# Kernel tuning notes

Hardware: AMD Instinct MI355X
Metric: run time of the kernel (lower is better)

Reference implementation:

```python
import jax, jax.numpy as jnp
import numpy as np

MIN_SPAN = 3
MAX_SPAN = 20
LEN_BONUS = 0.01
LN_EPS = 1e-5


def setup_inputs() -> dict:
    key = jax.random.key(0)
    ks = jax.random.split(key, 10)
    B, S, H = 16, 2048, 1024
    D = H // 2
    hidden_states = jax.random.normal(ks[0], (B, S, H), dtype=jnp.float32)
    lengths = jax.random.randint(ks[1], (B,), S // 2, S + 1)
    attention_mask = (jnp.arange(S)[None, :] < lengths[:, None]).astype(jnp.int32)
    return {
        'hidden_states': hidden_states,
        'attention_mask': attention_mask,
        'Wq': 0.02 * jax.random.normal(ks[2], (H, D), dtype=jnp.float32),
        'bq': jnp.zeros((D,), jnp.float32),
        'Wk': 0.02 * jax.random.normal(ks[3], (H, D), dtype=jnp.float32),
        'bk': jnp.zeros((D,), jnp.float32),
        'W1': 0.02 * jax.random.normal(ks[4], (H, D), dtype=jnp.float32),
        'b1': jnp.zeros((D,), jnp.float32),
        'ln_g': jnp.ones((D,), jnp.float32),
        'ln_b': jnp.zeros((D,), jnp.float32),
        'W2': 0.01 * jax.random.normal(ks[5], (D, 1), dtype=jnp.float32),
        'b2': jnp.zeros((1,), jnp.float32),
    }


def _token_scores(hidden_states, mask, Wq, bq, Wk, bk, W1, b1, ln_g, ln_b, W2, b2):
    q = hidden_states @ Wq + bq                      # [B,S,D]
    k = hidden_states @ Wk + bk                      # [B,S,D]
    d = q.shape[-1]
    scores = jnp.einsum('bsd,btd->bst', q, k) / jnp.sqrt(jnp.float32(d))
    scores = jnp.where(mask[:, None, :], scores, -10000.0)
    probs = jax.nn.softmax(scores, axis=-1)
    context = jnp.einsum('bst,bth->bsh', probs, hidden_states)  # [B,S,H]
    h = context @ W1 + b1
    mu = jnp.mean(h, axis=-1, keepdims=True)
    var = jnp.var(h, axis=-1, keepdims=True)
    h = (h - mu) * jax.lax.rsqrt(var + LN_EPS) * ln_g + ln_b
    h = jax.nn.relu(h)                               # dropout: eval mode -> identity
    ts = (h @ W2 + b2)[..., 0]                       # [B,S]
    return jnp.where(mask, ts, -10000.0)


def _rationale_mask(token_scores, mask):
    # Faithful to original: starts[0]==0 always, so prefix subtraction never
    # fires; span score = cumsum[start+L-1]/L + bonus. Argmax over (L asc, start asc)
    # with strict-greater updates == first max of the flattened (L, start) grid.
    B, S = token_scores.shape
    valid_len = jnp.sum(mask, axis=1)                # [B] int
    cum = jnp.cumsum(token_scores, axis=1)           # [B,S]
    L = jnp.arange(MIN_SPAN, MAX_SPAN + 1)           # [NL]
    starts = jnp.arange(S)                           # [S]
    end = jnp.clip(starts[None, :] + L[:, None] - 1, 0, S - 1)   # [NL,S]
    bonus = LEN_BONUS * (L.astype(jnp.float32) / MAX_SPAN)       # [NL]
    grid = cum[:, end] / L[None, :, None].astype(jnp.float32) + bonus[None, :, None]  # [B,NL,S]
    vl = valid_len[:, None, None]
    valid = (L[None, :, None] <= vl) & (starts[None, None, :] <= vl - L[None, :, None])
    grid = jnp.where(valid, grid, -jnp.inf)
    idx = jnp.argmax(grid.reshape(B, -1), axis=1)    # first max -> torch tie-break
    best_L = MIN_SPAN + idx // S
    best_s = idx % S
    pos = jnp.arange(S)[None, :]
    span = (pos >= best_s[:, None]) & (pos < (best_s + best_L)[:, None])
    short = (valid_len <= MIN_SPAN)[:, None]
    short_span = pos < valid_len[:, None]
    return jnp.where(short, short_span, span).astype(token_scores.dtype)


def reference(hidden_states, attention_mask, Wq, bq, Wk, bk, W1, b1, ln_g, ln_b, W2, b2):
    mask = attention_mask.astype(bool)
    token_scores = _token_scores(hidden_states, mask, Wq, bq, Wk, bk, W1, b1, ln_g, ln_b, W2, b2)
    rationale = _rationale_mask(token_scores, mask)
    token_probs = jax.nn.softmax(jnp.where(mask, token_scores, -10000.0), axis=-1)
    attended = hidden_states * rationale[:, :, None]
    lengths = jnp.sum(rationale, axis=1, keepdims=True) + 1e-6
    pooled = jnp.sum(attended, axis=1) / lengths
    return token_scores, rationale, token_probs, attended, pooled
```

## Files before the change

kernel.cpp:

```cpp
#include <hip/hip_runtime.h>

typedef _Float16 f16;
typedef __attribute__((ext_vector_type(8))) _Float16 f16x8;
typedef __attribute__((ext_vector_type(4))) _Float16 f16x4v;
typedef __attribute__((ext_vector_type(4))) float f32x4;

#define B_ 16
#define S_ 2048
#define H_ 1024
#define D_ 512

__device__ __forceinline__ void gload16(const f16* g, f16* l) {
  __builtin_amdgcn_global_load_lds(
      (const __attribute__((address_space(1))) unsigned int*)g,
      (__attribute__((address_space(3))) unsigned int*)l, 16, 0, 0);
}

__global__ __launch_bounds__(256) void cvt_hs_kernel(const float4* __restrict__ in,
                                                     f16x4v* __restrict__ out) {
  long long i = (long long)blockIdx.x * 256 + threadIdx.x;
  float4 v = in[i];
  f16x4v o = {(f16)v.x, (f16)v.y, (f16)v.z, (f16)v.w};
  out[i] = o;
}

__global__ __launch_bounds__(256) void build_wt_kernel(const float* __restrict__ Wq,
                                                       const float* __restrict__ Wk,
                                                       const float* __restrict__ W1,
                                                       f16* __restrict__ Wt) {
  int i = blockIdx.x * 256 + threadIdx.x;
  int n = i >> 10;
  int k = i & 1023;
  const float* src = (n < 512) ? Wq : ((n < 1024) ? Wk : W1);
  int nn = n & 511;
  Wt[i] = (f16)src[k * 512 + nn];
}

__global__ __launch_bounds__(256) void build_bias_kernel(const float* __restrict__ bq,
                                                         const float* __restrict__ bk,
                                                         float* __restrict__ bias) {
  int i = blockIdx.x * 256 + threadIdx.x;
  if (i < 1024) bias[i] = (i < 512) ? bq[i] : bk[i - 512];
}

__global__ __launch_bounds__(256) void lens_kernel(const int* __restrict__ mask,
                                                   int* __restrict__ lens) {
  int b = blockIdx.x;
  int tid = threadIdx.x;
  int s = 0;
  for (int c = tid; c < S_; c += 256) s += mask[b * S_ + c];
  __shared__ int r[256];
  r[tid] = s;
  __syncthreads();
  for (int o = 128; o > 0; o >>= 1) {
    if (tid < o) r[tid] += r[tid + o];
    __syncthreads();
  }
  if (tid == 0) lens[b] = r[0];
}

__global__ __launch_bounds__(256) void gemm_bt(
    const f16* __restrict__ A, const f16* __restrict__ Bm, void* __restrict__ Cout,
    int K, int lda, int ldb, int ldc,
    long long sA, long long sB, long long sC,
    float scale, const float* __restrict__ bias, int mode,
    const int* __restrict__ lens, int lflags) {
  const int bz = blockIdx.z;

  const int ntiles = gridDim.x, mtiles = gridDim.y;
  const int flat = blockIdx.y * ntiles + blockIdx.x;
  const int per = 8 * ntiles;
  const int grp = flat / per;
  const int rem = flat - grp * per;
  const int gbase = grp * 8;
  const int gsz = (mtiles - gbase) < 8 ? (mtiles - gbase) : 8;
  const int mt = gbase + rem % gsz;
  const int nt = rem / gsz;
  const int m0 = mt * 128;
  const int n0 = nt * 128;

  int Keff = K;
  if (lflags) {
    const int len = lens[(lflags & 1) ? (m0 >> 11) : bz];
    if ((lflags & 3) && (m0 & 2047) >= len) return;
    if ((lflags & 4) && n0 >= len) return;
    if (lflags & 8) { int kl = (len + 63) & ~63; Keff = kl < K ? kl : K; }
  }

  A += (long long)bz * sA;
  Bm += (long long)bz * sB;

  __shared__ f16 As[128 * 64];
  __shared__ f16 Bs[128 * 64];

  const int tid = threadIdx.x;
  const int lane = tid & 63;
  const int wid = tid >> 6;
  const int wm = wid & 1, wn = wid >> 1;

  f32x4 acc[4][4] = {};

  const int lr8 = lane >> 3;
  const int sg = lane & 7;

  for (int k0 = 0; k0 < Keff; k0 += 64) {
#pragma unroll
    for (int it = 0; it < 4; ++it) {
      const int r0 = it * 32 + wid * 8;
      const int r = r0 + lr8;
      const int cg = sg ^ (r & 7);
      gload16(A + (long long)(m0 + r) * lda + k0 + cg * 8, As + r0 * 64);
      gload16(Bm + (long long)(n0 + r) * ldb + k0 + cg * 8, Bs + r0 * 64);
    }
    __syncthreads();

#pragma unroll
    for (int kk = 0; kk < 64; kk += 32) {
      const int cg = (kk >> 3) + (lane >> 4);
      f16x8 af[4], bf[4];
#pragma unroll
      for (int i = 0; i < 4; ++i) {
        const int row = wm * 64 + i * 16 + (lane & 15);
        af[i] = *(const f16x8*)(As + row * 64 + ((cg ^ (row & 7)) << 3));
      }
#pragma unroll
      for (int j = 0; j < 4; ++j) {
        const int row = wn * 64 + j * 16 + (lane & 15);
        bf[j] = *(const f16x8*)(Bs + row * 64 + ((cg ^ (row & 7)) << 3));
      }
#pragma unroll
      for (int i = 0; i < 4; ++i)
#pragma unroll
        for (int j = 0; j < 4; ++j)
          acc[i][j] = __builtin_amdgcn_mfma_f32_16x16x32_f16(af[i], bf[j], acc[i][j], 0, 0, 0);
    }
    __syncthreads();
  }

  const long long cb = (long long)bz * sC;
  const int lr = ((lane >> 4) << 2);
  const int lc = lane & 15;
#pragma unroll
  for (int i = 0; i < 4; ++i) {
#pragma unroll
    for (int j = 0; j < 4; ++j) {
      const int col = n0 + wn * 64 + j * 16 + lc;
      const float bv = bias ? bias[col] : 0.0f;
      if (mode == 2) {
        const int rowb = m0 + wm * 64 + i * 16 + lr;
        const int b = rowb >> 11, t = rowb & 2047;
        f16x4v pk;
#pragma unroll
        for (int r = 0; r < 4; ++r) pk[r] = (f16)(acc[i][j][r] * scale + bv);
        *(f16x4v*)((f16*)Cout + ((long long)b << 20) + (long long)col * 2048 + t) = pk;
      } else {
#pragma unroll
        for (int r = 0; r < 4; ++r) {
          const int row = m0 + wm * 64 + i * 16 + lr + r;
          float v = acc[i][j][r] * scale + bv;
          if (mode == 1)
            ((f16*)Cout)[cb + (long long)row * ldc + col] = (f16)v;
          else
            ((float*)Cout)[cb + (long long)row * ldc + col] = v;
        }
      }
    }
  }
}

__global__ __launch_bounds__(256) void softmax_rows_kernel(f16* __restrict__ sc,
                                                           const int* __restrict__ lens) {
  const int tid = threadIdx.x;
  const int lane = tid & 63;
  const int row = blockIdx.x * 4 + (tid >> 6);
  const int len = lens[row >> 11];
  if ((row & 2047) >= ((len + 127) & ~127)) return;
  f16* p = sc + (long long)row * S_;

  f16x8 v[4];
#pragma unroll
  for (int c = 0; c < 4; ++c) v[c] = *(const f16x8*)(p + c * 512 + lane * 8);

  float m = -1e30f;
#pragma unroll
  for (int c = 0; c < 4; ++c)
#pragma unroll
    for (int j = 0; j < 8; ++j) {
      const int col = c * 512 + lane * 8 + j;
      if (col < len) m = fmaxf(m, (float)v[c][j]);
    }
#pragma unroll
  for (int o = 32; o > 0; o >>= 1) m = fmaxf(m, __shfl_xor(m, o, 64));

  float e[32];
  float s = 0.0f;
#pragma unroll
  for (int c = 0; c < 4; ++c)
#pragma unroll
    for (int j = 0; j < 8; ++j) {
      const int col = c * 512 + lane * 8 + j;
      const float x = (col < len) ? __expf((float)v[c][j] - m) : 0.0f;
      e[c * 8 + j] = x;
      s += x;
    }
#pragma unroll
  for (int o = 32; o > 0; o >>= 1) s += __shfl_xor(s, o, 64);
  const float inv = 1.0f / s;

#pragma unroll
  for (int c = 0; c < 4; ++c) {
    f16x8 w;
#pragma unroll
    for (int j = 0; j < 8; ++j) w[j] = (f16)(e[c * 8 + j] * inv);
    *(f16x8*)(p + c * 512 + lane * 8) = w;
  }
}

__global__ __launch_bounds__(256) void ln_score_kernel(
    const float* __restrict__ h, const int* __restrict__ lens,
    const float* __restrict__ g, const float* __restrict__ bt,
    const float* __restrict__ W2, const float* __restrict__ b2,
    float* __restrict__ ts, float* __restrict__ out_ts) {
  const int token = blockIdx.x;
  const float* hp = h + (long long)token * D_;
  const int tid = threadIdx.x;
  float x0 = hp[tid], x1 = hp[tid + 256];
  __shared__ float r1[256], r2[256];
  r1[tid] = x0 + x1;
  r2[tid] = x0 * x0 + x1 * x1;
  __syncthreads();
  for (int o = 128; o > 0; o >>= 1) {
    if (tid < o) { r1[tid] += r1[tid + o]; r2[tid] += r2[tid + o]; }
    __syncthreads();
  }
  const float mu = r1[0] * (1.0f / D_);
  const float var = r2[0] * (1.0f / D_) - mu * mu;
  const float rs = rsqrtf(var + 1e-5f);
  float y0 = fmaxf((x0 - mu) * rs * g[tid] + bt[tid], 0.0f);
  float y1 = fmaxf((x1 - mu) * rs * g[tid + 256] + bt[tid + 256], 0.0f);
  float d = y0 * W2[tid] + y1 * W2[tid + 256];
  __syncthreads();
  r1[tid] = d;
  __syncthreads();
  for (int o = 128; o > 0; o >>= 1) {
    if (tid < o) r1[tid] += r1[tid + o];
    __syncthreads();
  }
  if (tid == 0) {
    float v = r1[0] + b2[0];
    ts[token] = v;
    const int b = token >> 11, s = token & (S_ - 1);
    out_ts[token] = (s < lens[b]) ? v : -10000.0f;
  }
}

__global__ __launch_bounds__(256) void rationale_kernel(
    const float* __restrict__ ts, const int* __restrict__ lens,
    float* __restrict__ out_rat, int* __restrict__ span) {
  const int b = blockIdx.x;
  const int tid = threadIdx.x;
  const int len = lens[b];
  __shared__ float cum[S_];
  __shared__ float rbest[256];
  __shared__ int ridx[256];

  for (int s = tid; s < S_; s += 256)
    cum[s] = (s < len) ? ts[b * S_ + s] : -10000.0f;
  __syncthreads();
  if (tid == 0) {
    float a = 0.0f;
    for (int s = 0; s < S_; s += 4) {
      float4 v = *(float4*)(cum + s);
      a += v.x; v.x = a;
      a += v.y; v.y = a;
      a += v.z; v.z = a;
      a += v.w; v.w = a;
      *(float4*)(cum + s) = v;
    }
  }
  __syncthreads();

  float best = -3.4e38f;
  int bidx = 0x7fffffff;
  for (int idx = tid; idx < 18 * S_; idx += 256) {
    const int l = idx >> 11;
    const int s = idx & (S_ - 1);
    const int L = l + 3;
    if (L <= len && s <= len - L) {
      const float gv = cum[s + L - 1] / (float)L + 0.01f * ((float)L / 20.0f);
      if (gv > best) { best = gv; bidx = idx; }
    }
  }
  rbest[tid] = best;
  ridx[tid] = bidx;
  __syncthreads();
  for (int o = 128; o > 0; o >>= 1) {
    if (tid < o) {
      if (rbest[tid + o] > rbest[tid] ||
          (rbest[tid + o] == rbest[tid] && ridx[tid + o] < ridx[tid])) {
        rbest[tid] = rbest[tid + o];
        ridx[tid] = ridx[tid + o];
      }
    }
    __syncthreads();
  }
  const int bi = ridx[0];
  int start, sl;
  if (len <= 3) { start = 0; sl = len; }
  else { start = bi & (S_ - 1); sl = (bi >> 11) + 3; }
  if (tid == 0) { span[2 * b] = start; span[2 * b + 1] = sl; }
  for (int s = tid; s < S_; s += 256)
    out_rat[b * S_ + s] = (s >= start && s < start + sl) ? 1.0f : 0.0f;
}

__global__ __launch_bounds__(256) void tprobs_kernel(const float* __restrict__ ts,
                                                     const int* __restrict__ lens,
                                                     float* __restrict__ out) {
  const int b = blockIdx.x;
  const int tid = threadIdx.x;
  const int len = lens[b];
  const float* p = ts + b * S_;
  __shared__ float r[256];
  float m = -1e30f;
  for (int c = tid; c < len; c += 256) m = fmaxf(m, p[c]);
  r[tid] = m;
  __syncthreads();
  for (int o = 128; o > 0; o >>= 1) {
    if (tid < o) r[tid] = fmaxf(r[tid], r[tid + o]);
    __syncthreads();
  }
  m = r[0];
  __syncthreads();
  float s = 0.0f;
  for (int c = tid; c < len; c += 256) s += expf(p[c] - m);
  r[tid] = s;
  __syncthreads();
  for (int o = 128; o > 0; o >>= 1) {
    if (tid < o) r[tid] += r[tid + o];
    __syncthreads();
  }
  const float inv = 1.0f / r[0];
  for (int c = tid; c < S_; c += 256)
    out[b * S_ + c] = (c < len) ? expf(p[c] - m) * inv : 0.0f;
}

__global__ __launch_bounds__(256) void attended_kernel(const float4* __restrict__ hs,
                                                       const int* __restrict__ span,
                                                       float4* __restrict__ out) {
  long long i = (long long)blockIdx.x * 256 + threadIdx.x;
  const int token = (int)(i >> 8);
  const int b = token >> 11;
  const int s = token & (S_ - 1);
  const int st = span[2 * b], ln = span[2 * b + 1];
  float4 v = {0.0f, 0.0f, 0.0f, 0.0f};
  if (s >= st && s < st + ln) v = hs[i];
  out[i] = v;
}

__global__ __launch_bounds__(256) void pooled_kernel(const float* __restrict__ hs,
                                                     const int* __restrict__ span,
                                                     float* __restrict__ out) {
  const int b = blockIdx.x;
  const int tid = threadIdx.x;
  const int st = span[2 * b], ln = span[2 * b + 1];
  const float inv = 1.0f / ((float)ln + 1e-6f);
  for (int h = tid; h < H_; h += 256) {
    float s = 0.0f;
    for (int t = st; t < st + ln; ++t)
      s += hs[(long long)(b * S_ + t) * H_ + h];
    out[b * H_ + h] = s * inv;
  }
}

extern "C" void kernel_launch(void* const* d_in, const int* in_sizes, int n_in,
                              void* d_out, int out_size, void* d_ws, size_t ws_size,
                              hipStream_t stream) {
  const float* hs = (const float*)d_in[0];
  const int* amask = (const int*)d_in[1];
  const float* Wq = (const float*)d_in[2];
  const float* bq = (const float*)d_in[3];
  const float* Wk = (const float*)d_in[4];
  const float* bk = (const float*)d_in[5];
  const float* W1 = (const float*)d_in[6];
  const float* b1 = (const float*)d_in[7];
  const float* ln_g = (const float*)d_in[8];
  const float* ln_b = (const float*)d_in[9];
  const float* W2 = (const float*)d_in[10];
  const float* b2 = (const float*)d_in[11];

  float* out = (float*)d_out;
  char* ws = (char*)d_ws;

  const long long off_hs16 = 0;
  const long long off_qk = 67108864;
  const long long off_vt = 134217728;
  const long long off_wt = 167772160;
  const long long off_bias = 170917888;
  const long long off_ts = 170926080;
  const long long off_lens = 171057152;
  const long long off_span = 171057216;
  const long long off_scores = 171057408;

  f16* hs16 = (f16*)(ws + off_hs16);
  float* hbuf = (float*)(ws + off_hs16);
  f16* qk16 = (f16*)(ws + off_qk);
  f16* vt = (f16*)(ws + off_vt);
  f16* Wt = (f16*)(ws + off_wt);
  float* bias_qk = (float*)(ws + off_bias);
  float* ts = (float*)(ws + off_ts);
  int* lens = (int*)(ws + off_lens);
  int* span = (int*)(ws + off_span);
  f16* scores = (f16*)(ws + off_scores);

  const long long SC_PER_B = (long long)S_ * S_ * 2;
  int nb = 16;
  while (nb > 1 && off_scores + (long long)nb * SC_PER_B > (long long)ws_size) nb >>= 1;

  float* out_ts = out;
  float* out_rat = out + 32768;
  float* out_tp = out + 65536;
  float4* out_att = (float4*)(out + 98304);
  float* out_pool = out + 33652736;

  hipLaunchKernelGGL(lens_kernel, dim3(B_), dim3(256), 0, stream, amask, lens);
  hipLaunchKernelGGL(cvt_hs_kernel, dim3(32768), dim3(256), 0, stream,
                     (const float4*)hs, (f16x4v*)hs16);
  hipLaunchKernelGGL(build_wt_kernel, dim3(6144), dim3(256), 0, stream, Wq, Wk, W1, Wt);
  hipLaunchKernelGGL(build_bias_kernel, dim3(4), dim3(256), 0, stream, bq, bk, bias_qk);

  hipLaunchKernelGGL(gemm_bt, dim3(8, 256, 1), dim3(256), 0, stream,
                     hs16, Wt, (void*)qk16, 1024, 1024, 1024, 1024,
                     0LL, 0LL, 0LL, 1.0f, bias_qk, 1, lens, 1);
  hipLaunchKernelGGL(gemm_bt, dim3(4, 256, 1), dim3(256), 0, stream,
                     hs16, Wt + 1024 * 1024, (void*)vt, 1024, 1024, 1024, 2048,
                     0LL, 0LL, 0LL, 1.0f, b1, 2, lens, 1);

  const int chunks = 16 / nb;
  for (int c = 0; c < chunks; ++c) {
    const int b0 = c * nb;
    hipLaunchKernelGGL(gemm_bt, dim3(16, 16, nb), dim3(256), 0, stream,
                       qk16 + (long long)b0 * S_ * 1024,
                       qk16 + (long long)b0 * S_ * 1024 + 512,
                       (void*)scores, 512, 1024, 1024, 2048,
                       (long long)S_ * 1024, (long long)S_ * 1024, (long long)S_ * S_,
                       0.044194173824159216f , (const float*)nullptr, 1,
                       lens + b0, 2 | 4);
    hipLaunchKernelGGL(softmax_rows_kernel, dim3(nb * S_ / 4), dim3(256), 0, stream,
                       scores, lens + b0);
    hipLaunchKernelGGL(gemm_bt, dim3(4, 16, nb), dim3(256), 0, stream,
                       scores, vt + ((long long)b0 << 20),
                       (void*)(hbuf + (long long)b0 * S_ * D_), 2048, 2048, 2048, 512,
                       (long long)S_ * S_, 1LL << 20, (long long)S_ * D_,
                       1.0f, (const float*)nullptr, 0, lens + b0, 2 | 8);
  }

  hipLaunchKernelGGL(ln_score_kernel, dim3(B_ * S_), dim3(256), 0, stream,
                     hbuf, lens, ln_g, ln_b, W2, b2, ts, out_ts);

  hipLaunchKernelGGL(rationale_kernel, dim3(B_), dim3(256), 0, stream,
                     ts, lens, out_rat, span);
  hipLaunchKernelGGL(tprobs_kernel, dim3(B_), dim3(256), 0, stream, ts, lens, out_tp);
  hipLaunchKernelGGL(attended_kernel, dim3(32768), dim3(256), 0, stream,
                     (const float4*)hs, span, out_att);
  hipLaunchKernelGGL(pooled_kernel, dim3(B_), dim3(256), 0, stream, hs, span, out_pool);
}
```

Before: 729.2 us.

## Fuse setup kernels and QKV projections, skip padded work, tune launch bounds

```diff
diff --git a/kernel.cpp b/kernel.cpp
--- a/kernel.cpp
+++ b/kernel.cpp
@@ -24,56 +24,56 @@
   out[i] = o;
 }
 
-__global__ __launch_bounds__(256) void build_wt_kernel(const float* __restrict__ Wq,
-                                                       const float* __restrict__ Wk,
-                                                       const float* __restrict__ W1,
-                                                       f16* __restrict__ Wt) {
-  int i = blockIdx.x * 256 + threadIdx.x;
-  int n = i >> 10;
-  int k = i & 1023;
-  const float* src = (n < 512) ? Wq : ((n < 1024) ? Wk : W1);
-  int nn = n & 511;
-  Wt[i] = (f16)src[k * 512 + nn];
-}
-
-__global__ __launch_bounds__(256) void build_bias_kernel(const float* __restrict__ bq,
-                                                         const float* __restrict__ bk,
-                                                         float* __restrict__ bias) {
-  int i = blockIdx.x * 256 + threadIdx.x;
-  if (i < 1024) bias[i] = (i < 512) ? bq[i] : bk[i - 512];
-}
-
-__global__ __launch_bounds__(256) void lens_kernel(const int* __restrict__ mask,
-                                                   int* __restrict__ lens) {
-  int b = blockIdx.x;
-  int tid = threadIdx.x;
-  int s = 0;
-  for (int c = tid; c < S_; c += 256) s += mask[b * S_ + c];
-  __shared__ int r[256];
-  r[tid] = s;
-  __syncthreads();
-  for (int o = 128; o > 0; o >>= 1) {
-    if (tid < o) r[tid] += r[tid + o];
-    __syncthreads();
-  }
-  if (tid == 0) lens[b] = r[0];
-}
-
-__global__ __launch_bounds__(256) void gemm_bt(
+__global__ __launch_bounds__(256) void setup_kernel(
+    const float* __restrict__ Wq, const float* __restrict__ Wk,
+    const float* __restrict__ W1, const float* __restrict__ bq,
+    const float* __restrict__ bk, const float* __restrict__ b1,
+    const int* __restrict__ mask, f16* __restrict__ Wt,
+    float* __restrict__ bias, int* __restrict__ lens) {
+  const int blk = blockIdx.x;
+  const int tid = threadIdx.x;
+  if (blk < 6144) {
+    int i = blk * 256 + tid;
+    int n = i >> 10;
+    int k = i & 1023;
+    const float* src = (n < 512) ? Wq : ((n < 1024) ? Wk : W1);
+    Wt[i] = (f16)src[k * 512 + (n & 511)];
+  } else if (blk < 6150) {
+    int i = (blk - 6144) * 256 + tid;
+    if (i < 1536) bias[i] = (i < 512) ? bq[i] : ((i < 1024) ? bk[i - 512] : b1[i - 1024]);
+  } else {
+    int b = blk - 6150;
+    int s = 0;
+    for (int c = tid; c < S_; c += 256) s += mask[b * S_ + c];
+    __shared__ int r[256];
+    r[tid] = s;
+    __syncthreads();
+    for (int o = 128; o > 0; o >>= 1) {
+      if (tid < o) r[tid] += r[tid + o];
+      __syncthreads();
+    }
+    if (tid == 0) lens[b] = r[0];
+  }
+}
+
+template <int MW>
+__global__ __launch_bounds__(256, MW) void gemm_bt(
     const f16* __restrict__ A, const f16* __restrict__ Bm, void* __restrict__ Cout,
+    void* __restrict__ Cout2,
     int K, int lda, int ldb, int ldc,
     long long sA, long long sB, long long sC,
     float scale, const float* __restrict__ bias, int mode,
-    const int* __restrict__ lens, int lflags) {
+    const int* __restrict__ lens, int lflags, int mgrp) {
   const int bz = blockIdx.z;
 
   const int ntiles = gridDim.x, mtiles = gridDim.y;
   const int flat = blockIdx.y * ntiles + blockIdx.x;
-  const int per = 8 * ntiles;
+  const int per = mgrp * ntiles;
   const int grp = flat / per;
   const int rem = flat - grp * per;
-  const int gbase = grp * 8;
-  const int gsz = (mtiles - gbase) < 8 ? (mtiles - gbase) : 8;
+  const int gbase = grp * mgrp;
+  int gsz = mtiles - gbase;
+  if (gsz > mgrp) gsz = mgrp;
   const int mt = gbase + rem % gsz;
   const int nt = rem / gsz;
   const int m0 = mt * 128;
@@ -146,22 +146,24 @@
     for (int j = 0; j < 4; ++j) {
       const int col = n0 + wn * 64 + j * 16 + lc;
       const float bv = bias ? bias[col] : 0.0f;
-      if (mode == 2) {
+      if (mode == 2 || (mode == 3 && col >= 1024)) {
         const int rowb = m0 + wm * 64 + i * 16 + lr;
         const int b = rowb >> 11, t = rowb & 2047;
+        const int d = (mode == 3) ? (col - 1024) : col;
+        f16* dst = (f16*)((mode == 3) ? Cout2 : Cout);
         f16x4v pk;
 #pragma unroll
         for (int r = 0; r < 4; ++r) pk[r] = (f16)(acc[i][j][r] * scale + bv);
-        *(f16x4v*)((f16*)Cout + ((long long)b << 20) + (long long)col * 2048 + t) = pk;
+        *(f16x4v*)(dst + ((long long)b << 20) + (long long)d * 2048 + t) = pk;
       } else {
 #pragma unroll
         for (int r = 0; r < 4; ++r) {
           const int row = m0 + wm * 64 + i * 16 + lr + r;
           float v = acc[i][j][r] * scale + bv;
-          if (mode == 1)
+          if (mode == 0)
+            ((float*)Cout)[cb + (long long)row * ldc + col] = v;
+          else
             ((f16*)Cout)[cb + (long long)row * ldc + col] = (f16)v;
-          else
-            ((float*)Cout)[cb + (long long)row * ldc + col] = v;
         }
       }
     }
@@ -174,28 +176,33 @@
   const int lane = tid & 63;
   const int row = blockIdx.x * 4 + (tid >> 6);
   const int len = lens[row >> 11];
-  if ((row & 2047) >= ((len + 127) & ~127)) return;
+  const int cl = (len + 127) & ~127;
+  if ((row & 2047) >= cl) return;
   f16* p = sc + (long long)row * S_;
 
   f16x8 v[4];
 #pragma unroll
-  for (int c = 0; c < 4; ++c) v[c] = *(const f16x8*)(p + c * 512 + lane * 8);
+  for (int c = 0; c < 4; ++c)
+    if (c * 512 < cl) v[c] = *(const f16x8*)(p + c * 512 + lane * 8);
 
   float m = -1e30f;
 #pragma unroll
-  for (int c = 0; c < 4; ++c)
+  for (int c = 0; c < 4; ++c) {
+    if (c * 512 >= cl) continue;
 #pragma unroll
     for (int j = 0; j < 8; ++j) {
       const int col = c * 512 + lane * 8 + j;
       if (col < len) m = fmaxf(m, (float)v[c][j]);
     }
+  }
 #pragma unroll
   for (int o = 32; o > 0; o >>= 1) m = fmaxf(m, __shfl_xor(m, o, 64));
 
   float e[32];
   float s = 0.0f;
 #pragma unroll
-  for (int c = 0; c < 4; ++c)
+  for (int c = 0; c < 4; ++c) {
+    if (c * 512 >= cl) continue;
 #pragma unroll
     for (int j = 0; j < 8; ++j) {
       const int col = c * 512 + lane * 8 + j;
@@ -203,12 +210,14 @@
       e[c * 8 + j] = x;
       s += x;
     }
+  }
 #pragma unroll
   for (int o = 32; o > 0; o >>= 1) s += __shfl_xor(s, o, 64);
   const float inv = 1.0f / s;
 
 #pragma unroll
   for (int c = 0; c < 4; ++c) {
+    if (c * 512 >= cl) continue;
     f16x8 w;
 #pragma unroll
     for (int j = 0; j < 8; ++j) w[j] = (f16)(e[c * 8 + j] * inv);
@@ -222,8 +231,13 @@
     const float* __restrict__ W2, const float* __restrict__ b2,
     float* __restrict__ ts, float* __restrict__ out_ts) {
   const int token = blockIdx.x;
+  const int tid = threadIdx.x;
+  const int b = token >> 11, s = token & (S_ - 1);
+  if (s >= lens[b]) {
+    if (tid == 0) { ts[token] = -10000.0f; out_ts[token] = -10000.0f; }
+    return;
+  }
   const float* hp = h + (long long)token * D_;
-  const int tid = threadIdx.x;
   float x0 = hp[tid], x1 = hp[tid + 256];
   __shared__ float r1[256], r2[256];
   r1[tid] = x0 + x1;
@@ -249,8 +263,7 @@
   if (tid == 0) {
     float v = r1[0] + b2[0];
     ts[token] = v;
-    const int b = token >> 11, s = token & (S_ - 1);
-    out_ts[token] = (s < lens[b]) ? v : -10000.0f;
+    out_ts[token] = v;
   }
 }
 
@@ -406,7 +419,7 @@
   f16* qk16 = (f16*)(ws + off_qk);
   f16* vt = (f16*)(ws + off_vt);
   f16* Wt = (f16*)(ws + off_wt);
-  float* bias_qk = (float*)(ws + off_bias);
+  float* bias_full = (float*)(ws + off_bias);
   float* ts = (float*)(ws + off_ts);
   int* lens = (int*)(ws + off_lens);
   int* span = (int*)(ws + off_span);
@@ -422,45 +435,36 @@
   float4* out_att = (float4*)(out + 98304);
   float* out_pool = out + 33652736;
 
-  hipLaunchKernelGGL(lens_kernel, dim3(B_), dim3(256), 0, stream, amask, lens);
-  hipLaunchKernelGGL(cvt_hs_kernel, dim3(32768), dim3(256), 0, stream,
-                     (const float4*)hs, (f16x4v*)hs16);
-  hipLaunchKernelGGL(build_wt_kernel, dim3(6144), dim3(256), 0, stream, Wq, Wk, W1, Wt);
-  hipLaunchKernelGGL(build_bias_kernel, dim3(4), dim3(256), 0, stream, bq, bk, bias_qk);
-
-  hipLaunchKernelGGL(gemm_bt, dim3(8, 256, 1), dim3(256), 0, stream,
-                     hs16, Wt, (void*)qk16, 1024, 1024, 1024, 1024,
-                     0LL, 0LL, 0LL, 1.0f, bias_qk, 1, lens, 1);
-  hipLaunchKernelGGL(gemm_bt, dim3(4, 256, 1), dim3(256), 0, stream,
-                     hs16, Wt + 1024 * 1024, (void*)vt, 1024, 1024, 1024, 2048,
-                     0LL, 0LL, 0LL, 1.0f, b1, 2, lens, 1);
+  setup_kernel<<<dim3(6166), dim3(256), 0, stream>>>(Wq, Wk, W1, bq, bk, b1, amask,
+                                                     Wt, bias_full, lens);
+  cvt_hs_kernel<<<dim3(32768), dim3(256), 0, stream>>>((const float4*)hs, (f16x4v*)hs16);
+
+  gemm_bt<2><<<dim3(12, 256, 1), dim3(256), 0, stream>>>(
+      hs16, Wt, (void*)qk16, (void*)vt, 1024, 1024, 1024, 1024,
+      0LL, 0LL, 0LL, 1.0f, bias_full, 3, lens, 1, 8);
 
   const int chunks = 16 / nb;
   for (int c = 0; c < chunks; ++c) {
     const int b0 = c * nb;
-    hipLaunchKernelGGL(gemm_bt, dim3(16, 16, nb), dim3(256), 0, stream,
-                       qk16 + (long long)b0 * S_ * 1024,
-                       qk16 + (long long)b0 * S_ * 1024 + 512,
-                       (void*)scores, 512, 1024, 1024, 2048,
-                       (long long)S_ * 1024, (long long)S_ * 1024, (long long)S_ * S_,
-                       0.044194173824159216f , (const float*)nullptr, 1,
-                       lens + b0, 2 | 4);
-    hipLaunchKernelGGL(softmax_rows_kernel, dim3(nb * S_ / 4), dim3(256), 0, stream,
-                       scores, lens + b0);
-    hipLaunchKernelGGL(gemm_bt, dim3(4, 16, nb), dim3(256), 0, stream,
-                       scores, vt + ((long long)b0 << 20),
-                       (void*)(hbuf + (long long)b0 * S_ * D_), 2048, 2048, 2048, 512,
-                       (long long)S_ * S_, 1LL << 20, (long long)S_ * D_,
-                       1.0f, (const float*)nullptr, 0, lens + b0, 2 | 8);
-  }
-
-  hipLaunchKernelGGL(ln_score_kernel, dim3(B_ * S_), dim3(256), 0, stream,
-                     hbuf, lens, ln_g, ln_b, W2, b2, ts, out_ts);
-
-  hipLaunchKernelGGL(rationale_kernel, dim3(B_), dim3(256), 0, stream,
-                     ts, lens, out_rat, span);
-  hipLaunchKernelGGL(tprobs_kernel, dim3(B_), dim3(256), 0, stream, ts, lens, out_tp);
-  hipLaunchKernelGGL(attended_kernel, dim3(32768), dim3(256), 0, stream,
-                     (const float4*)hs, span, out_att);
-  hipLaunchKernelGGL(pooled_kernel, dim3(B_), dim3(256), 0, stream, hs, span, out_pool);
-}
+    gemm_bt<4><<<dim3(16, 16, nb), dim3(256), 0, stream>>>(
+        qk16 + (long long)b0 * S_ * 1024,
+        qk16 + (long long)b0 * S_ * 1024 + 512,
+        (void*)scores, (void*)nullptr, 512, 1024, 1024, 2048,
+        (long long)S_ * 1024, (long long)S_ * 1024, (long long)S_ * S_,
+        0.044194173824159216f , (const float*)nullptr, 1,
+        lens + b0, 2 | 4, 8);
+    softmax_rows_kernel<<<dim3(nb * S_ / 4), dim3(256), 0, stream>>>(scores, lens + b0);
+    gemm_bt<4><<<dim3(4, 16, nb), dim3(256), 0, stream>>>(
+        scores, vt + ((long long)b0 << 20),
+        (void*)(hbuf + (long long)b0 * S_ * D_), (void*)nullptr, 2048, 2048, 2048, 512,
+        (long long)S_ * S_, 1LL << 20, (long long)S_ * D_,
+        1.0f, (const float*)nullptr, 0, lens + b0, 2 | 8, 1);
+  }
+
+  ln_score_kernel<<<dim3(B_ * S_), dim3(256), 0, stream>>>(hbuf, lens, ln_g, ln_b,
+                                                           W2, b2, ts, out_ts);
+  rationale_kernel<<<dim3(B_), dim3(256), 0, stream>>>(ts, lens, out_rat, span);
+  tprobs_kernel<<<dim3(B_), dim3(256), 0, stream>>>(ts, lens, out_tp);
+  attended_kernel<<<dim3(32768), dim3(256), 0, stream>>>((const float4*)hs, span, out_att);
+  pooled_kernel<<<dim3(B_), dim3(256), 0, stream>>>(hs, span, out_pool);
+}
```

Measured after the change: 667.6 us. -8.5%, faster.
